# Optimization experiments

Measured on AMD Instinct MI355X. Metric: run time of the kernel, lower is better.

The kernel has to match this reference:

```python
import jax, jax.numpy as jnp
import numpy as np

N_ENT, N_REL, B, D = 100000, 500, 16, 128
P_NORM = 1
EPS = 1e-12


def _l2_normalize(x):
    # mirrors torch.nn.functional.normalize(x, 2, -1)
    n = jnp.sqrt(jnp.sum(x * x, axis=-1, keepdims=True))
    return x / jnp.maximum(n, EPS)


def setup_inputs() -> dict:
    key = jax.random.key(0)
    k0, k1, k2, k3 = jax.random.split(key, 4)
    # xavier_normal_ init: std = sqrt(2 / (fan_in + fan_out))
    ent_emb = jax.random.normal(k0, (N_ENT, D), dtype=jnp.float32) * np.sqrt(2.0 / (N_ENT + D))
    rel_emb = jax.random.normal(k1, (N_REL, D), dtype=jnp.float32) * np.sqrt(2.0 / (N_REL + D))
    e1 = jax.random.randint(k2, (B,), 0, N_ENT, dtype=jnp.int64)
    rel = jax.random.randint(k3, (B,), 0, N_REL, dtype=jnp.int64)
    X = jnp.zeros((B, D), dtype=jnp.float32)   # unused by forward (as in source)
    A = jnp.zeros((B, B), dtype=jnp.float32)   # unused by forward (as in source)
    return {"e1": e1, "rel": rel, "X": X, "A": A, "ent_emb": ent_emb, "rel_emb": rel_emb}


def reference(e1, rel, X, A, ent_emb, rel_emb) -> jnp.ndarray:
    # e1_embedded = normalize(ent_emb[e1]); rel_embedded = normalize(rel_emb[rel])
    e1_e = _l2_normalize(ent_emb[e1])          # [B, D]
    rel_e = _l2_normalize(rel_emb[rel])        # [B, D]
    node = _l2_normalize(ent_emb)              # [N, D]
    head_add_rel = e1_e + rel_e                # [B, D]
    # broadcast pairwise difference: [B, N, D]
    diff = head_add_rel[:, None, :] - node[None, :, :]
    if P_NORM == 1:
        dist = jnp.sum(jnp.abs(diff), axis=2)              # [B, N]
    else:
        dist = jnp.sum(jnp.abs(diff) ** P_NORM, axis=2) ** (1.0 / P_NORM)
    # loss_name == 'BCELoss' -> softmax over entities
    pred = jax.nn.softmax(dist, axis=-1)       # [B, N]
    return pred
```

## Files before the change

kernel.cpp:

```cpp
#include <hip/hip_runtime.h>
#include <hip/hip_bf16.h>

#define N_ENT 100000
#define NB 16
#define DIM 128
#define TILE 64
#define RSTRIDE 132
#define NBLK 1024
#define N_TILES ((N_ENT + TILE - 1) / TILE)

__global__ __launch_bounds__(128) void head_kernel(
    const int* __restrict__ e1, const int* __restrict__ rel,
    const float* __restrict__ ent, const float* __restrict__ relemb,
    float* __restrict__ head)
{
    int b = blockIdx.x, d = threadIdx.x;
    float ev = ent[e1[b] * DIM + d];
    float rv = relemb[rel[b] * DIM + d];
    __shared__ float s1[DIM], s2[DIM];
    s1[d] = ev * ev;
    s2[d] = rv * rv;
    __syncthreads();
    for (int s = 64; s > 0; s >>= 1) {
        if (d < s) { s1[d] += s1[d + s]; s2[d] += s2[d + s]; }
        __syncthreads();
    }
    float ne = fmaxf(sqrtf(s1[0]), 1e-12f);
    float nr = fmaxf(sqrtf(s2[0]), 1e-12f);
    head[b * DIM + d] = ev / ne + rv / nr;
}

__global__ __launch_bounds__(256) void dist_kernel(
    const float* __restrict__ ent, const float* __restrict__ head,
    float* __restrict__ partials, float* __restrict__ out)
{
    __shared__ float ldsRow[TILE * RSTRIDE];
    __shared__ float ldsInv[TILE];

    const int tid  = threadIdx.x;
    const int lane = tid & 63;
    const int wv   = __builtin_amdgcn_readfirstlane(tid >> 6);
    const int bbase = wv * 4;
    const float4* __restrict__ hg = (const float4*)head;

    float es0 = 0.f, es1 = 0.f, es2 = 0.f, es3 = 0.f;

    for (int tile = blockIdx.x; tile < N_TILES; tile += NBLK) {
        const int n0 = tile * TILE;
        __syncthreads();

        {
            const float4* eg = (const float4*)ent;
            #pragma unroll
            for (int i = 0; i < 8; i++) {
                int g = tid + i * 256;
                int r = g >> 5, c = g & 31;
                int gr = n0 + r;
                if (gr >= N_ENT) gr = N_ENT - 1;
                float4 v = eg[gr * (DIM / 4) + c];
                *(float4*)&ldsRow[r * RSTRIDE + c * 4] = v;
            }
        }
        __syncthreads();

        {
            int r = tid >> 2, q = tid & 3;
            const float* p = &ldsRow[r * RSTRIDE + q * 32];
            float s = 0.f;
            #pragma unroll
            for (int k = 0; k < 8; k++) {
                float4 v = *(const float4*)&p[k * 4];
                s = fmaf(v.x, v.x, s); s = fmaf(v.y, v.y, s);
                s = fmaf(v.z, v.z, s); s = fmaf(v.w, v.w, s);
            }
            s += __shfl_down(s, 2);
            s += __shfl_down(s, 1);
            if (q == 0) ldsInv[r] = 1.0f / fmaxf(sqrtf(s), 1e-12f);
        }
        __syncthreads();

        const float inv = ldsInv[lane];
        const float* rp = &ldsRow[lane * RSTRIDE];

        float a0 = 0.f, a1 = 0.f, a2 = 0.f, a3 = 0.f;
        #pragma unroll 8
        for (int j = 0; j < DIM / 4; j++) {
            float4 v  = *(const float4*)&rp[j * 4];
            float4 q0 = hg[(bbase + 0) * (DIM / 4) + j];
            float4 q1 = hg[(bbase + 1) * (DIM / 4) + j];
            float4 q2 = hg[(bbase + 2) * (DIM / 4) + j];
            float4 q3 = hg[(bbase + 3) * (DIM / 4) + j];
            a0 += fabsf(fmaf(-v.x, inv, q0.x)) + fabsf(fmaf(-v.y, inv, q0.y))
                + fabsf(fmaf(-v.z, inv, q0.z)) + fabsf(fmaf(-v.w, inv, q0.w));
            a1 += fabsf(fmaf(-v.x, inv, q1.x)) + fabsf(fmaf(-v.y, inv, q1.y))
                + fabsf(fmaf(-v.z, inv, q1.z)) + fabsf(fmaf(-v.w, inv, q1.w));
            a2 += fabsf(fmaf(-v.x, inv, q2.x)) + fabsf(fmaf(-v.y, inv, q2.y))
                + fabsf(fmaf(-v.z, inv, q2.z)) + fabsf(fmaf(-v.w, inv, q2.w));
            a3 += fabsf(fmaf(-v.x, inv, q3.x)) + fabsf(fmaf(-v.y, inv, q3.y))
                + fabsf(fmaf(-v.z, inv, q3.z)) + fabsf(fmaf(-v.w, inv, q3.w));
        }

        const int n = n0 + lane;
        const bool valid = (n < N_ENT);
        float e0 = valid ? __expf(a0) : 0.f;
        float e1 = valid ? __expf(a1) : 0.f;
        float e2 = valid ? __expf(a2) : 0.f;
        float e3 = valid ? __expf(a3) : 0.f;
        if (valid) {
            out[(bbase + 0) * N_ENT + n] = e0;
            out[(bbase + 1) * N_ENT + n] = e1;
            out[(bbase + 2) * N_ENT + n] = e2;
            out[(bbase + 3) * N_ENT + n] = e3;
        }
        es0 += e0; es1 += e1; es2 += e2; es3 += e3;
    }

#define WRED(x) { x += __shfl_down(x, 32); x += __shfl_down(x, 16); \
                  x += __shfl_down(x, 8);  x += __shfl_down(x, 4);  \
                  x += __shfl_down(x, 2);  x += __shfl_down(x, 1); }
    WRED(es0) WRED(es1) WRED(es2) WRED(es3)
#undef WRED
    if (lane == 0) {
        partials[(bbase + 0) * NBLK + blockIdx.x] = es0;
        partials[(bbase + 1) * NBLK + blockIdx.x] = es1;
        partials[(bbase + 2) * NBLK + blockIdx.x] = es2;
        partials[(bbase + 3) * NBLK + blockIdx.x] = es3;
    }
}

__global__ __launch_bounds__(256) void scale_kernel(
    float* __restrict__ out, const float* __restrict__ partials)
{
    const int b = blockIdx.y;
    const int tid = threadIdx.x;

    const int i = blockIdx.x * 256 + tid;
    float4 v = make_float4(0.f, 0.f, 0.f, 0.f);
    float4* row = (float4*)&out[b * N_ENT];
    const bool valid = (i < N_ENT / 4);
    if (valid) v = row[i];

    float s = 0.f;
    #pragma unroll
    for (int k = 0; k < NBLK / 256; k++) s += partials[b * NBLK + k * 256 + tid];
    s += __shfl_down(s, 32); s += __shfl_down(s, 16);
    s += __shfl_down(s, 8);  s += __shfl_down(s, 4);
    s += __shfl_down(s, 2);  s += __shfl_down(s, 1);
    __shared__ float red[4];
    if ((tid & 63) == 0) red[tid >> 6] = s;
    __syncthreads();
    const float invS = 1.0f / (red[0] + red[1] + red[2] + red[3]);

    if (valid) {
        v.x *= invS; v.y *= invS; v.z *= invS; v.w *= invS;
        row[i] = v;
    }
}

extern "C" void kernel_launch(void* const* d_in, const int* in_sizes, int n_in,
                              void* d_out, int out_size, void* d_ws, size_t ws_size,
                              hipStream_t stream) {
    const int*   e1     = (const int*)d_in[0];
    const int*   rel    = (const int*)d_in[1];
    const float* ent    = (const float*)d_in[4];
    const float* relemb = (const float*)d_in[5];
    float* out = (float*)d_out;

    float* head     = (float*)d_ws;
    float* partials = (float*)((char*)d_ws + 8192);

    head_kernel<<<16, 128, 0, stream>>>(e1, rel, ent, relemb, head);
    dist_kernel<<<NBLK, 256, 0, stream>>>(ent, head, partials, out);
    scale_kernel<<<dim3((N_ENT / 4 + 255) / 256, NB), 256, 0, stream>>>(out, partials);
}
```

Baseline: 113.3 us.

## Fuse softmax normalization into distance kernel via grid-wide atomic barrier

Removes the separate scale kernel: each block keeps its exp values in registers (two tiles per block), publishes partial sums, and uses atomic counters as a grid-wide barrier. The first 16 blocks reduce the row sums, and every block then writes normalized outputs directly. This saves a full read and write pass over the 16x100000 output and one kernel launch. In exchange it adds a memset, spin-waits that assume all 1024 blocks are co-resident (launch bounds raised to 4 blocks per SM), and a guard timeout that could silently give wrong results if that residency does not hold.

```diff
diff --git a/kernel.cpp b/kernel.cpp
--- a/kernel.cpp
+++ b/kernel.cpp
@@ -8,6 +8,7 @@
 #define RSTRIDE 132
 #define NBLK 1024
 #define N_TILES ((N_ENT + TILE - 1) / TILE)
+#define SCOPE __HIP_MEMORY_SCOPE_AGENT
 
 __global__ __launch_bounds__(128) void head_kernel(
     const int* __restrict__ e1, const int* __restrict__ rel,
@@ -30,12 +31,14 @@
     head[b * DIM + d] = ev / ne + rv / nr;
 }
 
-__global__ __launch_bounds__(256) void dist_kernel(
+__global__ __launch_bounds__(256, 4) void dist_kernel(
     const float* __restrict__ ent, const float* __restrict__ head,
-    float* __restrict__ partials, float* __restrict__ out)
+    float* partials, float* rowsum, unsigned* cnt1, unsigned* flag2,
+    float* __restrict__ out)
 {
     __shared__ float ldsRow[TILE * RSTRIDE];
     __shared__ float ldsInv[TILE];
+    __shared__ float ldsRed[4];
 
     const int tid  = threadIdx.x;
     const int lane = tid & 63;
@@ -43,9 +46,16 @@
     const int bbase = wv * 4;
     const float4* __restrict__ hg = (const float4*)head;
 
+    float ex[2][4];
     float es0 = 0.f, es1 = 0.f, es2 = 0.f, es3 = 0.f;
 
-    for (int tile = blockIdx.x; tile < N_TILES; tile += NBLK) {
+    #pragma unroll
+    for (int t = 0; t < 2; t++) {
+        const int tile = blockIdx.x + t * NBLK;
+        if (tile >= N_TILES) {
+            ex[t][0] = ex[t][1] = ex[t][2] = ex[t][3] = 0.f;
+            continue;
+        }
         const int n0 = tile * TILE;
         __syncthreads();
 
@@ -100,18 +110,12 @@
                 + fabsf(fmaf(-v.z, inv, q3.z)) + fabsf(fmaf(-v.w, inv, q3.w));
         }
 
-        const int n = n0 + lane;
-        const bool valid = (n < N_ENT);
+        const bool valid = (n0 + lane) < N_ENT;
         float e0 = valid ? __expf(a0) : 0.f;
         float e1 = valid ? __expf(a1) : 0.f;
         float e2 = valid ? __expf(a2) : 0.f;
         float e3 = valid ? __expf(a3) : 0.f;
-        if (valid) {
-            out[(bbase + 0) * N_ENT + n] = e0;
-            out[(bbase + 1) * N_ENT + n] = e1;
-            out[(bbase + 2) * N_ENT + n] = e2;
-            out[(bbase + 3) * N_ENT + n] = e3;
-        }
+        ex[t][0] = e0; ex[t][1] = e1; ex[t][2] = e2; ex[t][3] = e3;
         es0 += e0; es1 += e1; es2 += e2; es3 += e3;
     }
 
@@ -121,39 +125,73 @@
     WRED(es0) WRED(es1) WRED(es2) WRED(es3)
 #undef WRED
     if (lane == 0) {
-        partials[(bbase + 0) * NBLK + blockIdx.x] = es0;
-        partials[(bbase + 1) * NBLK + blockIdx.x] = es1;
-        partials[(bbase + 2) * NBLK + blockIdx.x] = es2;
-        partials[(bbase + 3) * NBLK + blockIdx.x] = es3;
-    }
-}
-
-__global__ __launch_bounds__(256) void scale_kernel(
-    float* __restrict__ out, const float* __restrict__ partials)
-{
-    const int b = blockIdx.y;
-    const int tid = threadIdx.x;
-
-    const int i = blockIdx.x * 256 + tid;
-    float4 v = make_float4(0.f, 0.f, 0.f, 0.f);
-    float4* row = (float4*)&out[b * N_ENT];
-    const bool valid = (i < N_ENT / 4);
-    if (valid) v = row[i];
-
-    float s = 0.f;
+        __hip_atomic_store(&partials[(bbase + 0) * NBLK + blockIdx.x], es0, __ATOMIC_RELEASE, SCOPE);
+        __hip_atomic_store(&partials[(bbase + 1) * NBLK + blockIdx.x], es1, __ATOMIC_RELEASE, SCOPE);
+        __hip_atomic_store(&partials[(bbase + 2) * NBLK + blockIdx.x], es2, __ATOMIC_RELEASE, SCOPE);
+        __hip_atomic_store(&partials[(bbase + 3) * NBLK + blockIdx.x], es3, __ATOMIC_RELEASE, SCOPE);
+    }
+    __syncthreads();
+    if (tid == 0)
+        __hip_atomic_fetch_add(&cnt1[blockIdx.x & 7], 1u, __ATOMIC_ACQ_REL, SCOPE);
+
+    if (blockIdx.x < NB) {
+        if (tid == 0) {
+            long guard = 0;
+            for (;;) {
+                unsigned s = 0;
+                #pragma unroll
+                for (int i = 0; i < 8; i++)
+                    s += __hip_atomic_load(&cnt1[i], __ATOMIC_ACQUIRE, SCOPE);
+                if (s >= NBLK) break;
+                __builtin_amdgcn_s_sleep(2);
+                if (++guard > (1L << 22)) break;
+            }
+        }
+        __syncthreads();
+        const int b = blockIdx.x;
+        float s = 0.f;
+        for (int k = tid; k < NBLK; k += 256)
+            s += __hip_atomic_load(&partials[b * NBLK + k], __ATOMIC_RELAXED, SCOPE);
+        s += __shfl_down(s, 32); s += __shfl_down(s, 16);
+        s += __shfl_down(s, 8);  s += __shfl_down(s, 4);
+        s += __shfl_down(s, 2);  s += __shfl_down(s, 1);
+        if (lane == 0) ldsRed[wv] = s;
+        __syncthreads();
+        if (tid == 0) {
+            float tot = ldsRed[0] + ldsRed[1] + ldsRed[2] + ldsRed[3];
+            __hip_atomic_store(&rowsum[b], tot, __ATOMIC_RELEASE, SCOPE);
+            __hip_atomic_fetch_add(flag2, 1u, __ATOMIC_ACQ_REL, SCOPE);
+        }
+    }
+
+    if (tid == 0) {
+        long guard = 0;
+        while (__hip_atomic_load(flag2, __ATOMIC_ACQUIRE, SCOPE) < NB) {
+            __builtin_amdgcn_s_sleep(2);
+            if (++guard > (1L << 22)) break;
+        }
+    }
+    __syncthreads();
+
+    float sv = 0.f;
+    if (lane < 4)
+        sv = __hip_atomic_load(&rowsum[bbase + lane], __ATOMIC_RELAXED, SCOPE);
+    const float i0 = 1.0f / __shfl(sv, 0);
+    const float i1 = 1.0f / __shfl(sv, 1);
+    const float i2 = 1.0f / __shfl(sv, 2);
+    const float i3 = 1.0f / __shfl(sv, 3);
+
     #pragma unroll
-    for (int k = 0; k < NBLK / 256; k++) s += partials[b * NBLK + k * 256 + tid];
-    s += __shfl_down(s, 32); s += __shfl_down(s, 16);
-    s += __shfl_down(s, 8);  s += __shfl_down(s, 4);
-    s += __shfl_down(s, 2);  s += __shfl_down(s, 1);
-    __shared__ float red[4];
-    if ((tid & 63) == 0) red[tid >> 6] = s;
-    __syncthreads();
-    const float invS = 1.0f / (red[0] + red[1] + red[2] + red[3]);
-
-    if (valid) {
-        v.x *= invS; v.y *= invS; v.z *= invS; v.w *= invS;
-        row[i] = v;
+    for (int t = 0; t < 2; t++) {
+        const int tile = blockIdx.x + t * NBLK;
+        if (tile >= N_TILES) continue;
+        const int n = tile * TILE + lane;
+        if (n < N_ENT) {
+            out[(bbase + 0) * N_ENT + n] = ex[t][0] * i0;
+            out[(bbase + 1) * N_ENT + n] = ex[t][1] * i1;
+            out[(bbase + 2) * N_ENT + n] = ex[t][2] * i2;
+            out[(bbase + 3) * N_ENT + n] = ex[t][3] * i3;
+        }
     }
 }
 
@@ -166,10 +204,15 @@
     const float* relemb = (const float*)d_in[5];
     float* out = (float*)d_out;
 
-    float* head     = (float*)d_ws;
-    float* partials = (float*)((char*)d_ws + 8192);
+    float*    head     = (float*)d_ws;
+    float*    partials = (float*)((char*)d_ws + 8192);
+    float*    rowsum   = (float*)((char*)d_ws + 73728);
+    unsigned* cnt1     = (unsigned*)((char*)d_ws + 73792);
+    unsigned* flag2    = (unsigned*)((char*)d_ws + 73824);
+
+    hipMemsetAsync((char*)d_ws + 73792, 0, 36, stream);
 
     head_kernel<<<16, 128, 0, stream>>>(e1, rel, ent, relemb, head);
-    dist_kernel<<<NBLK, 256, 0, stream>>>(ent, head, partials, out);
-    scale_kernel<<<dim3((N_ENT / 4 + 255) / 256, NB), 256, 0, stream>>>(out, partials);
+    dist_kernel<<<NBLK, 256, 0, stream>>>(ent, head, partials, rowsum,
+                                          cnt1, flag2, out);
 }
```

Result: slower. 406.8 us (+258.9%).

## Use one tile per block with two waves each handling eight queries

Applied to the files above, without the earlier changes.

The dist kernel no longer loops persistently over tiles. It launches one 128-thread block per 64-entity tile, and each wave computes eight query rows instead of four, so every LDS row read is reused across more queries. Partial sums are now written per tile, and the scale kernel loops over all tiles to reduce them. This drops the persistent-loop barriers and the fixed block count, but it launches about 1563 small blocks and makes each scale block reduce a larger partials array.

```diff
diff --git a/kernel.cpp b/kernel.cpp
--- a/kernel.cpp
+++ b/kernel.cpp
@@ -6,7 +6,6 @@
 #define DIM 128
 #define TILE 64
 #define RSTRIDE 132
-#define NBLK 1024
 #define N_TILES ((N_ENT + TILE - 1) / TILE)
 
 __global__ __launch_bounds__(128) void head_kernel(
@@ -30,7 +29,7 @@
     head[b * DIM + d] = ev / ne + rv / nr;
 }
 
-__global__ __launch_bounds__(256) void dist_kernel(
+__global__ __launch_bounds__(128) void dist_kernel(
     const float* __restrict__ ent, const float* __restrict__ head,
     float* __restrict__ partials, float* __restrict__ out)
 {
@@ -40,91 +39,72 @@
     const int tid  = threadIdx.x;
     const int lane = tid & 63;
     const int wv   = __builtin_amdgcn_readfirstlane(tid >> 6);
-    const int bbase = wv * 4;
+    const int bbase = wv * 8;
+    const int n0 = blockIdx.x * TILE;
     const float4* __restrict__ hg = (const float4*)head;
 
-    float es0 = 0.f, es1 = 0.f, es2 = 0.f, es3 = 0.f;
+    {
+        const float4* eg = (const float4*)ent;
+        #pragma unroll
+        for (int i = 0; i < 16; i++) {
+            int g = tid + i * 128;
+            int r = g >> 5, c = g & 31;
+            int gr = n0 + r;
+            if (gr >= N_ENT) gr = N_ENT - 1;
+            float4 v = eg[gr * (DIM / 4) + c];
+            *(float4*)&ldsRow[r * RSTRIDE + c * 4] = v;
+        }
+    }
+    __syncthreads();
 
-    for (int tile = blockIdx.x; tile < N_TILES; tile += NBLK) {
-        const int n0 = tile * TILE;
-        __syncthreads();
+    {
+        int r = tid >> 1, q = tid & 1;
+        const float* p = &ldsRow[r * RSTRIDE + q * 64];
+        float s = 0.f;
+        #pragma unroll
+        for (int k = 0; k < 16; k++) {
+            float4 v = *(const float4*)&p[k * 4];
+            s = fmaf(v.x, v.x, s); s = fmaf(v.y, v.y, s);
+            s = fmaf(v.z, v.z, s); s = fmaf(v.w, v.w, s);
+        }
+        s += __shfl_down(s, 1);
+        if (q == 0) ldsInv[r] = 1.0f / fmaxf(sqrtf(s), 1e-12f);
+    }
+    __syncthreads();
 
-        {
-            const float4* eg = (const float4*)ent;
-            #pragma unroll
-            for (int i = 0; i < 8; i++) {
-                int g = tid + i * 256;
-                int r = g >> 5, c = g & 31;
-                int gr = n0 + r;
-                if (gr >= N_ENT) gr = N_ENT - 1;
-                float4 v = eg[gr * (DIM / 4) + c];
-                *(float4*)&ldsRow[r * RSTRIDE + c * 4] = v;
-            }
+    const float inv = ldsInv[lane];
+    const float* rp = &ldsRow[lane * RSTRIDE];
+
+    float acc[8];
+    #pragma unroll
+    for (int b = 0; b < 8; b++) acc[b] = 0.f;
+
+    for (int j = 0; j < DIM / 4; j++) {
+        float4 v = *(const float4*)&rp[j * 4];
+        #pragma unroll
+        for (int b = 0; b < 8; b++) {
+            float4 h = hg[(bbase + b) * (DIM / 4) + j];
+            acc[b] += fabsf(fmaf(-v.x, inv, h.x)) + fabsf(fmaf(-v.y, inv, h.y))
+                    + fabsf(fmaf(-v.z, inv, h.z)) + fabsf(fmaf(-v.w, inv, h.w));
         }
-        __syncthreads();
-
-        {
-            int r = tid >> 2, q = tid & 3;
-            const float* p = &ldsRow[r * RSTRIDE + q * 32];
-            float s = 0.f;
-            #pragma unroll
-            for (int k = 0; k < 8; k++) {
-                float4 v = *(const float4*)&p[k * 4];
-                s = fmaf(v.x, v.x, s); s = fmaf(v.y, v.y, s);
-                s = fmaf(v.z, v.z, s); s = fmaf(v.w, v.w, s);
-            }
-            s += __shfl_down(s, 2);
-            s += __shfl_down(s, 1);
-            if (q == 0) ldsInv[r] = 1.0f / fmaxf(sqrtf(s), 1e-12f);
-        }
-        __syncthreads();
-
-        const float inv = ldsInv[lane];
-        const float* rp = &ldsRow[lane * RSTRIDE];
-
-        float a0 = 0.f, a1 = 0.f, a2 = 0.f, a3 = 0.f;
-        #pragma unroll 8
-        for (int j = 0; j < DIM / 4; j++) {
-            float4 v  = *(const float4*)&rp[j * 4];
-            float4 q0 = hg[(bbase + 0) * (DIM / 4) + j];
-            float4 q1 = hg[(bbase + 1) * (DIM / 4) + j];
-            float4 q2 = hg[(bbase + 2) * (DIM / 4) + j];
-            float4 q3 = hg[(bbase + 3) * (DIM / 4) + j];
-            a0 += fabsf(fmaf(-v.x, inv, q0.x)) + fabsf(fmaf(-v.y, inv, q0.y))
-                + fabsf(fmaf(-v.z, inv, q0.z)) + fabsf(fmaf(-v.w, inv, q0.w));
-            a1 += fabsf(fmaf(-v.x, inv, q1.x)) + fabsf(fmaf(-v.y, inv, q1.y))
-                + fabsf(fmaf(-v.z, inv, q1.z)) + fabsf(fmaf(-v.w, inv, q1.w));
-            a2 += fabsf(fmaf(-v.x, inv, q2.x)) + fabsf(fmaf(-v.y, inv, q2.y))
-                + fabsf(fmaf(-v.z, inv, q2.z)) + fabsf(fmaf(-v.w, inv, q2.w));
-            a3 += fabsf(fmaf(-v.x, inv, q3.x)) + fabsf(fmaf(-v.y, inv, q3.y))
-                + fabsf(fmaf(-v.z, inv, q3.z)) + fabsf(fmaf(-v.w, inv, q3.w));
-        }
-
-        const int n = n0 + lane;
-        const bool valid = (n < N_ENT);
-        float e0 = valid ? __expf(a0) : 0.f;
-        float e1 = valid ? __expf(a1) : 0.f;
-        float e2 = valid ? __expf(a2) : 0.f;
-        float e3 = valid ? __expf(a3) : 0.f;
-        if (valid) {
-            out[(bbase + 0) * N_ENT + n] = e0;
-            out[(bbase + 1) * N_ENT + n] = e1;
-            out[(bbase + 2) * N_ENT + n] = e2;
-            out[(bbase + 3) * N_ENT + n] = e3;
-        }
-        es0 += e0; es1 += e1; es2 += e2; es3 += e3;
     }
 
-#define WRED(x) { x += __shfl_down(x, 32); x += __shfl_down(x, 16); \
-                  x += __shfl_down(x, 8);  x += __shfl_down(x, 4);  \
-                  x += __shfl_down(x, 2);  x += __shfl_down(x, 1); }
-    WRED(es0) WRED(es1) WRED(es2) WRED(es3)
-#undef WRED
-    if (lane == 0) {
-        partials[(bbase + 0) * NBLK + blockIdx.x] = es0;
-        partials[(bbase + 1) * NBLK + blockIdx.x] = es1;
-        partials[(bbase + 2) * NBLK + blockIdx.x] = es2;
-        partials[(bbase + 3) * NBLK + blockIdx.x] = es3;
+    const int n = n0 + lane;
+    const bool valid = (n < N_ENT);
+    float e[8];
+    #pragma unroll
+    for (int b = 0; b < 8; b++) {
+        e[b] = valid ? __expf(acc[b]) : 0.f;
+        if (valid) out[(bbase + b) * N_ENT + n] = e[b];
+    }
+
+    #pragma unroll
+    for (int b = 0; b < 8; b++) {
+        float s = e[b];
+        s += __shfl_down(s, 32); s += __shfl_down(s, 16);
+        s += __shfl_down(s, 8);  s += __shfl_down(s, 4);
+        s += __shfl_down(s, 2);  s += __shfl_down(s, 1);
+        if (lane == 0) partials[(bbase + b) * N_TILES + blockIdx.x] = s;
     }
 }
 
@@ -141,8 +121,7 @@
     if (valid) v = row[i];
 
     float s = 0.f;
-    #pragma unroll
-    for (int k = 0; k < NBLK / 256; k++) s += partials[b * NBLK + k * 256 + tid];
+    for (int k = tid; k < N_TILES; k += 256) s += partials[b * N_TILES + k];
     s += __shfl_down(s, 32); s += __shfl_down(s, 16);
     s += __shfl_down(s, 8);  s += __shfl_down(s, 4);
     s += __shfl_down(s, 2);  s += __shfl_down(s, 1);
@@ -170,6 +149,6 @@
     float* partials = (float*)((char*)d_ws + 8192);
 
     head_kernel<<<16, 128, 0, stream>>>(e1, rel, ent, relemb, head);
-    dist_kernel<<<NBLK, 256, 0, stream>>>(ent, head, partials, out);
+    dist_kernel<<<N_TILES, 128, 0, stream>>>(ent, head, partials, out);
     scale_kernel<<<dim3((N_ENT / 4 + 255) / 256, NB), 256, 0, stream>>>(out, partials);
 }
```

Measured after the change: 126.3 us. 1.11x slower.

## Launch one block per tile and hold head vectors in registers via readlane

Applied to the files above, without the earlier changes.

The distance kernel drops the grid-stride loop and launches one block per 64-entity tile, giving 1563 blocks instead of 1024 persistent blocks. Each lane now loads one float4 slice of its wave's four head vectors into registers once. The inner loop broadcasts the needed elements with readlane instead of reloading them from global memory on every iteration. The scale kernel reads a variable number of per-block partial sums. This trades cached global loads for scalar readlane ops and more register pressure from the fully unrolled loop, and it adds block-launch overhead and more partials to reduce.

```diff
diff --git a/kernel.cpp b/kernel.cpp
--- a/kernel.cpp
+++ b/kernel.cpp
@@ -6,8 +6,11 @@
 #define DIM 128
 #define TILE 64
 #define RSTRIDE 132
-#define NBLK 1024
 #define N_TILES ((N_ENT + TILE - 1) / TILE)
+
+__device__ __forceinline__ float rdlane(float x, int l) {
+    return __int_as_float(__builtin_amdgcn_readlane(__float_as_int(x), l));
+}
 
 __global__ __launch_bounds__(128) void head_kernel(
     const int* __restrict__ e1, const int* __restrict__ rel,
@@ -41,90 +44,93 @@
     const int lane = tid & 63;
     const int wv   = __builtin_amdgcn_readfirstlane(tid >> 6);
     const int bbase = wv * 4;
-    const float4* __restrict__ hg = (const float4*)head;
+    const int n0 = blockIdx.x * TILE;
 
-    float es0 = 0.f, es1 = 0.f, es2 = 0.f, es3 = 0.f;
+    const float4* hg = (const float4*)head;
+    const int Lc = lane & 31;
+    float4 H0 = hg[(bbase + 0) * 32 + Lc];
+    float4 H1 = hg[(bbase + 1) * 32 + Lc];
+    float4 H2 = hg[(bbase + 2) * 32 + Lc];
+    float4 H3 = hg[(bbase + 3) * 32 + Lc];
 
-    for (int tile = blockIdx.x; tile < N_TILES; tile += NBLK) {
-        const int n0 = tile * TILE;
-        __syncthreads();
+    {
+        const float4* eg = (const float4*)ent;
+        #pragma unroll
+        for (int i = 0; i < 8; i++) {
+            int g = tid + i * 256;
+            int r = g >> 5, c = g & 31;
+            int gr = n0 + r;
+            if (gr >= N_ENT) gr = N_ENT - 1;
+            float4 v = eg[gr * (DIM / 4) + c];
+            *(float4*)&ldsRow[r * RSTRIDE + c * 4] = v;
+        }
+    }
+    __syncthreads();
 
-        {
-            const float4* eg = (const float4*)ent;
-            #pragma unroll
-            for (int i = 0; i < 8; i++) {
-                int g = tid + i * 256;
-                int r = g >> 5, c = g & 31;
-                int gr = n0 + r;
-                if (gr >= N_ENT) gr = N_ENT - 1;
-                float4 v = eg[gr * (DIM / 4) + c];
-                *(float4*)&ldsRow[r * RSTRIDE + c * 4] = v;
-            }
+    {
+        int r = tid >> 2, q = tid & 3;
+        const float* p = &ldsRow[r * RSTRIDE + q * 32];
+        float s = 0.f;
+        #pragma unroll
+        for (int k = 0; k < 8; k++) {
+            float4 v = *(const float4*)&p[k * 4];
+            s = fmaf(v.x, v.x, s); s = fmaf(v.y, v.y, s);
+            s = fmaf(v.z, v.z, s); s = fmaf(v.w, v.w, s);
         }
-        __syncthreads();
+        s += __shfl_down(s, 2);
+        s += __shfl_down(s, 1);
+        if (q == 0) ldsInv[r] = 1.0f / fmaxf(sqrtf(s), 1e-12f);
+    }
+    __syncthreads();
 
-        {
-            int r = tid >> 2, q = tid & 3;
-            const float* p = &ldsRow[r * RSTRIDE + q * 32];
-            float s = 0.f;
-            #pragma unroll
-            for (int k = 0; k < 8; k++) {
-                float4 v = *(const float4*)&p[k * 4];
-                s = fmaf(v.x, v.x, s); s = fmaf(v.y, v.y, s);
-                s = fmaf(v.z, v.z, s); s = fmaf(v.w, v.w, s);
-            }
-            s += __shfl_down(s, 2);
-            s += __shfl_down(s, 1);
-            if (q == 0) ldsInv[r] = 1.0f / fmaxf(sqrtf(s), 1e-12f);
-        }
-        __syncthreads();
+    const float inv = ldsInv[lane];
+    const float* rp = &ldsRow[lane * RSTRIDE];
 
-        const float inv = ldsInv[lane];
-        const float* rp = &ldsRow[lane * RSTRIDE];
+    float a0 = 0.f, a1 = 0.f, a2 = 0.f, a3 = 0.f;
+    #pragma unroll
+    for (int j = 0; j < DIM / 4; j++) {
+        float4 v = *(const float4*)&rp[j * 4];
+        a0 += fabsf(fmaf(-v.x, inv, rdlane(H0.x, j)))
+            + fabsf(fmaf(-v.y, inv, rdlane(H0.y, j)))
+            + fabsf(fmaf(-v.z, inv, rdlane(H0.z, j)))
+            + fabsf(fmaf(-v.w, inv, rdlane(H0.w, j)));
+        a1 += fabsf(fmaf(-v.x, inv, rdlane(H1.x, j)))
+            + fabsf(fmaf(-v.y, inv, rdlane(H1.y, j)))
+            + fabsf(fmaf(-v.z, inv, rdlane(H1.z, j)))
+            + fabsf(fmaf(-v.w, inv, rdlane(H1.w, j)));
+        a2 += fabsf(fmaf(-v.x, inv, rdlane(H2.x, j)))
+            + fabsf(fmaf(-v.y, inv, rdlane(H2.y, j)))
+            + fabsf(fmaf(-v.z, inv, rdlane(H2.z, j)))
+            + fabsf(fmaf(-v.w, inv, rdlane(H2.w, j)));
+        a3 += fabsf(fmaf(-v.x, inv, rdlane(H3.x, j)))
+            + fabsf(fmaf(-v.y, inv, rdlane(H3.y, j)))
+            + fabsf(fmaf(-v.z, inv, rdlane(H3.z, j)))
+            + fabsf(fmaf(-v.w, inv, rdlane(H3.w, j)));
+    }
 
-        float a0 = 0.f, a1 = 0.f, a2 = 0.f, a3 = 0.f;
-        #pragma unroll 8
-        for (int j = 0; j < DIM / 4; j++) {
-            float4 v  = *(const float4*)&rp[j * 4];
-            float4 q0 = hg[(bbase + 0) * (DIM / 4) + j];
-            float4 q1 = hg[(bbase + 1) * (DIM / 4) + j];
-            float4 q2 = hg[(bbase + 2) * (DIM / 4) + j];
-            float4 q3 = hg[(bbase + 3) * (DIM / 4) + j];
-            a0 += fabsf(fmaf(-v.x, inv, q0.x)) + fabsf(fmaf(-v.y, inv, q0.y))
-                + fabsf(fmaf(-v.z, inv, q0.z)) + fabsf(fmaf(-v.w, inv, q0.w));
-            a1 += fabsf(fmaf(-v.x, inv, q1.x)) + fabsf(fmaf(-v.y, inv, q1.y))
-                + fabsf(fmaf(-v.z, inv, q1.z)) + fabsf(fmaf(-v.w, inv, q1.w));
-            a2 += fabsf(fmaf(-v.x, inv, q2.x)) + fabsf(fmaf(-v.y, inv, q2.y))
-                + fabsf(fmaf(-v.z, inv, q2.z)) + fabsf(fmaf(-v.w, inv, q2.w));
-            a3 += fabsf(fmaf(-v.x, inv, q3.x)) + fabsf(fmaf(-v.y, inv, q3.y))
-                + fabsf(fmaf(-v.z, inv, q3.z)) + fabsf(fmaf(-v.w, inv, q3.w));
-        }
-
-        const int n = n0 + lane;
-        const bool valid = (n < N_ENT);
-        float e0 = valid ? __expf(a0) : 0.f;
-        float e1 = valid ? __expf(a1) : 0.f;
-        float e2 = valid ? __expf(a2) : 0.f;
-        float e3 = valid ? __expf(a3) : 0.f;
-        if (valid) {
-            out[(bbase + 0) * N_ENT + n] = e0;
-            out[(bbase + 1) * N_ENT + n] = e1;
-            out[(bbase + 2) * N_ENT + n] = e2;
-            out[(bbase + 3) * N_ENT + n] = e3;
-        }
-        es0 += e0; es1 += e1; es2 += e2; es3 += e3;
+    const int n = n0 + lane;
+    const bool valid = (n < N_ENT);
+    float e0 = valid ? __expf(a0) : 0.f;
+    float e1 = valid ? __expf(a1) : 0.f;
+    float e2 = valid ? __expf(a2) : 0.f;
+    float e3 = valid ? __expf(a3) : 0.f;
+    if (valid) {
+        out[(bbase + 0) * N_ENT + n] = e0;
+        out[(bbase + 1) * N_ENT + n] = e1;
+        out[(bbase + 2) * N_ENT + n] = e2;
+        out[(bbase + 3) * N_ENT + n] = e3;
     }
 
 #define WRED(x) { x += __shfl_down(x, 32); x += __shfl_down(x, 16); \
                   x += __shfl_down(x, 8);  x += __shfl_down(x, 4);  \
                   x += __shfl_down(x, 2);  x += __shfl_down(x, 1); }
-    WRED(es0) WRED(es1) WRED(es2) WRED(es3)
+    WRED(e0) WRED(e1) WRED(e2) WRED(e3)
 #undef WRED
     if (lane == 0) {
-        partials[(bbase + 0) * NBLK + blockIdx.x] = es0;
-        partials[(bbase + 1) * NBLK + blockIdx.x] = es1;
-        partials[(bbase + 2) * NBLK + blockIdx.x] = es2;
-        partials[(bbase + 3) * NBLK + blockIdx.x] = es3;
+        partials[(bbase + 0) * N_TILES + blockIdx.x] = e0;
+        partials[(bbase + 1) * N_TILES + blockIdx.x] = e1;
+        partials[(bbase + 2) * N_TILES + blockIdx.x] = e2;
+        partials[(bbase + 3) * N_TILES + blockIdx.x] = e3;
     }
 }
 
@@ -141,8 +147,7 @@
     if (valid) v = row[i];
 
     float s = 0.f;
-    #pragma unroll
-    for (int k = 0; k < NBLK / 256; k++) s += partials[b * NBLK + k * 256 + tid];
+    for (int k = tid; k < N_TILES; k += 256) s += partials[b * N_TILES + k];
     s += __shfl_down(s, 32); s += __shfl_down(s, 16);
     s += __shfl_down(s, 8);  s += __shfl_down(s, 4);
     s += __shfl_down(s, 2);  s += __shfl_down(s, 1);
@@ -170,6 +175,6 @@
     float* partials = (float*)((char*)d_ws + 8192);
 
     head_kernel<<<16, 128, 0, stream>>>(e1, rel, ent, relemb, head);
-    dist_kernel<<<NBLK, 256, 0, stream>>>(ent, head, partials, out);
+    dist_kernel<<<N_TILES, 256, 0, stream>>>(ent, head, partials, out);
     scale_kernel<<<dim3((N_ENT / 4 + 255) / 256, NB), 256, 0, stream>>>(out, partials);
 }
```

Result: no change. 114.6 us (+1.1%).
